# Optimization experiments

Hardware: AMD Instinct MI355X
Metric: run time of the kernel (lower is better)

## Reference

```python
import jax, jax.numpy as jnp
import numpy as np

G, C_PER, C_IN, J, B, H, W, K = 8, 32, 256, 64, 16, 56, 56, 3


def setup_inputs() -> dict:
    key = jax.random.key(0)
    kx, kw, kb = jax.random.split(key, 3)
    x = jax.random.normal(kx, (B, C_IN, H, W), dtype=jnp.float32)
    # Per-cluster conv weights [G, j_rank, c, K, K] and biases [G, j_rank]
    weight = jax.random.normal(kw, (G, J, C_PER, K, K), dtype=jnp.float32) * 0.05
    bias = jax.random.normal(kb, (G, J), dtype=jnp.float32) * 0.01
    # Arrangements: 8 clusters of 32 non-contiguous channel indices (fixed permutation)
    arrangements = jnp.asarray(
        np.random.RandomState(0).permutation(C_IN).reshape(G, C_PER), dtype=jnp.int32
    )
    return {"x": x, "weight": weight, "bias": bias, "arrangements": arrangements}


def reference(x, weight, bias, arrangements):
    # Gather channel subsets: x[:, arr] -> [B, G, c, H, W] -> [G, B, c, H, W]
    xg = jnp.transpose(x[:, arrangements], (1, 0, 2, 3, 4))

    def conv1(xi, wi):
        # xi: [B, c, H, W], wi: [J, c, K, K]; stride 1, pad 1, dilation 1 (torch default cross-correlation)
        return jax.lax.conv_general_dilated(
            xi, wi,
            window_strides=(1, 1),
            padding=((1, 1), (1, 1)),
            dimension_numbers=("NCHW", "OIHW", "NCHW"),
        )

    out = jax.vmap(conv1)(xg, weight)              # [G, B, J, H, W]
    out = out + bias[:, None, :, None, None]
    g, b, j, h, w = out.shape
    # torch.cat(dim=1) over clusters -> [B, G*J, H, W]
    return jnp.transpose(out, (1, 0, 2, 3, 4)).reshape(b, g * j, h, w)
```

## Files before the change

kernel.cpp:

```cpp
#include <hip/hip_runtime.h>


#define NG 8
#define CPER 32
#define CIN 256
#define NJ 64
#define NB 16
#define NH 56
#define NW 56
#define HW (NH * NW)
#define PLANE_DW 236
#define SLOT_DW 944
#define NSLOT 6
#define BUF_DW (NSLOT * SLOT_DW)
#define NTASK 336

typedef __attribute__((ext_vector_type(8))) short short8v;
typedef __attribute__((ext_vector_type(4))) float float4v;
typedef __attribute__((ext_vector_type(4))) unsigned int uint4v;

__device__ __forceinline__ unsigned bf16rne(float f) {
    unsigned u = __float_as_uint(f);
    return (u + 0x7FFFu + ((u >> 16) & 1u)) >> 16;
}

#define MFMA __builtin_amdgcn_mfma_f32_16x16x32_bf16

__global__ __launch_bounds__(256)
void transpose_w(const float* __restrict__ w, unsigned short* __restrict__ wt) {
    const int idx = blockIdx.x * 256 + threadIdx.x;
    const float* src = w + (size_t)idx * 9;
    const int g = idx >> 11, jc = idx & 2047;
    #pragma unroll
    for (int t = 0; t < 9; ++t)
        wt[(g * 9 + t) * 2048 + jc] = (unsigned short)bf16rne(src[t]);
}

__global__ __launch_bounds__(256, 4)
void gconv_mfma(const float* __restrict__ x,
                const unsigned short* __restrict__ wt,
                const float* __restrict__ bias,
                const int* __restrict__ arr,
                float* __restrict__ out) {
    __shared__ __align__(16) unsigned int smw[BUF_DW];

    const int tid   = threadIdx.x;
    const int chunk = blockIdx.x;
    const int b     = blockIdx.y;
    const int g     = blockIdx.z;
    const int lane  = tid & 63;
    const int jt    = tid >> 6;
    const int n     = lane & 15;
    const int kq    = lane >> 4;
    const int rbase = chunk * 4;

    short8v A[9];
    {
        const unsigned short* wl =
            wt + (size_t)(g * 9) * 2048 + (jt * 16 + n) * CPER + kq * 8;
        #pragma unroll
        for (int t = 0; t < 9; ++t)
            A[t] = *(const short8v*)(wl + t * 2048);
    }
    float4v binit;
    #pragma unroll
    for (int i = 0; i < 4; ++i) binit[i] = bias[g * NJ + jt * 16 + kq * 4 + i];

    if (tid < 48) {
        int lr = tid >> 3, rm = tid & 7;
        int q = rm >> 1, px = (rm & 1) ? 57 : 0;
        uint4v z = {0u, 0u, 0u, 0u};
        *(uint4v*)(smw + lr * SLOT_DW + q * PLANE_DW + px * 4) = z;
    }

    const float* xb = x + (size_t)b * (CIN * HW);
    const int* ag = arr + g * CPER;
    auto stage = [&](int t) {
        int q = t & 3, s = t >> 2;
        int p4 = s % 14, lr = s / 14;
        int irow = rbase - 1 + lr;
        bool v = (unsigned)irow < NH;
        const float* src = xb + irow * NW + 4 * p4;
        float4v vv[8];
        #pragma unroll
        for (int j = 0; j < 8; ++j) {
            float4v t0 = {0.f, 0.f, 0.f, 0.f};
            if (v) t0 = *(const float4v*)(src + ag[8 * q + j] * HW);
            vv[j] = t0;
        }
        unsigned int* d = smw + lr * SLOT_DW + q * PLANE_DW + (1 + 4 * p4) * 4;
        #pragma unroll
        for (int i = 0; i < 4; ++i) {
            uint4v val;
            #pragma unroll
            for (int dd = 0; dd < 4; ++dd)
                val[dd] = bf16rne(vv[2 * dd][i]) | (bf16rne(vv[2 * dd + 1][i]) << 16);
            *(uint4v*)(d + 4 * i) = val;
        }
    };
    stage(tid);
    if (tid < NTASK - 256) stage(tid + 256);
    __syncthreads();

    const int ob = ((b * (NG * NJ) + g * NJ + jt * 16 + kq * 4) * NH + rbase) * NW;
    int rl = 0, col = n;
    #pragma unroll
    for (int tp = 0; tp < 7; ++tp) {
        const int rlA = rl, colA = col;
        col += 16; if (col >= NW) { col -= NW; ++rl; }
        const int rlB = rl, colB = col;
        col += 16; if (col >= NW) { col -= NW; ++rl; }
        const unsigned int* pA = smw + rlA * SLOT_DW + kq * PLANE_DW + colA * 4;
        const unsigned int* pB = smw + rlB * SLOT_DW + kq * PLANE_DW + colB * 4;
        float4v a0 = binit, a1 = binit;
        #pragma unroll
        for (int kh = 0; kh < 3; ++kh)
            #pragma unroll
            for (int kw = 0; kw < 3; ++kw) {
                short8v x0 = *(const short8v*)(pA + kh * SLOT_DW + kw * 4);
                short8v y0 = *(const short8v*)(pB + kh * SLOT_DW + kw * 4);
                a0 = MFMA(A[kh * 3 + kw], x0, a0, 0, 0, 0);
                a1 = MFMA(A[kh * 3 + kw], y0, a1, 0, 0, 0);
            }
        const int oA = ob + rlA * NW + colA;
        const int oB = ob + rlB * NW + colB;
        #pragma unroll
        for (int i = 0; i < 4; ++i) {
            out[oA + i * HW] = a0[i];
            out[oB + i * HW] = a1[i];
        }
    }
}

extern "C" void kernel_launch(void* const* d_in, const int* in_sizes, int n_in,
                              void* d_out, int out_size, void* d_ws, size_t ws_size,
                              hipStream_t stream) {
    const float* x    = (const float*)d_in[0];
    const float* wght = (const float*)d_in[1];
    const float* bias = (const float*)d_in[2];
    const int*   arr  = (const int*)d_in[3];
    float* out = (float*)d_out;
    unsigned short* wtp = (unsigned short*)d_ws;

    transpose_w<<<dim3(64), 256, 0, stream>>>(wght, wtp);
    dim3 grid(14, NB, NG);
    gconv_mfma<<<grid, 256, 0, stream>>>(x, wtp, bias, arr, out);
}
```

Before: 169.3 us.

## Split waves over two output-channel tiles and two row halves for B-fragment reuse

Each wave now computes two 16-channel output tiles for half of the block's pixels (2 rows × 56), instead of one channel tile for all 4 rows. Every LDS-loaded input fragment now feeds two MFMAs, which halves shared-memory read traffic per MFMA. In exchange each wave holds twice the weight registers (18 short8 fragments) and four accumulators, which raises VGPR pressure and may hurt occupancy under launch_bounds(256,4). A tail step handles the seventh 16-pixel tile of each half.

```diff
diff --git a/kernel.cpp b/kernel.cpp
--- a/kernel.cpp
+++ b/kernel.cpp
@@ -49,22 +49,28 @@
     const int b     = blockIdx.y;
     const int g     = blockIdx.z;
     const int lane  = tid & 63;
-    const int jt    = tid >> 6;
+    const int wid   = tid >> 6;
     const int n     = lane & 15;
     const int kq    = lane >> 4;
+    const int jt0   = (wid & 1) * 2;
+    const int ph    = wid >> 1;
     const int rbase = chunk * 4;
 
-    short8v A[9];
-    {
+    short8v A[2][9];
+    #pragma unroll
+    for (int jj = 0; jj < 2; ++jj) {
         const unsigned short* wl =
-            wt + (size_t)(g * 9) * 2048 + (jt * 16 + n) * CPER + kq * 8;
+            wt + (size_t)(g * 9) * 2048 + ((jt0 + jj) * 16 + n) * CPER + kq * 8;
         #pragma unroll
         for (int t = 0; t < 9; ++t)
-            A[t] = *(const short8v*)(wl + t * 2048);
+            A[jj][t] = *(const short8v*)(wl + t * 2048);
     }
-    float4v binit;
+    float4v binit[2];
     #pragma unroll
-    for (int i = 0; i < 4; ++i) binit[i] = bias[g * NJ + jt * 16 + kq * 4 + i];
+    for (int jj = 0; jj < 2; ++jj)
+        #pragma unroll
+        for (int i = 0; i < 4; ++i)
+            binit[jj][i] = bias[g * NJ + (jt0 + jj) * 16 + kq * 4 + i];
 
     if (tid < 48) {
         int lr = tid >> 3, rm = tid & 7;
@@ -102,33 +108,55 @@
     if (tid < NTASK - 256) stage(tid + 256);
     __syncthreads();
 
-    const int ob = ((b * (NG * NJ) + g * NJ + jt * 16 + kq * 4) * NH + rbase) * NW;
-    int rl = 0, col = n;
+    const int ob0 = ((b * (NG * NJ) + g * NJ + jt0 * 16 + kq * 4) * NH + rbase) * NW;
+    const int ob1 = ob0 + 16 * HW;
+    int rl = 2 * ph, col = n;
     #pragma unroll
-    for (int tp = 0; tp < 7; ++tp) {
+    for (int tp = 0; tp < 3; ++tp) {
         const int rlA = rl, colA = col;
         col += 16; if (col >= NW) { col -= NW; ++rl; }
         const int rlB = rl, colB = col;
         col += 16; if (col >= NW) { col -= NW; ++rl; }
         const unsigned int* pA = smw + rlA * SLOT_DW + kq * PLANE_DW + colA * 4;
         const unsigned int* pB = smw + rlB * SLOT_DW + kq * PLANE_DW + colB * 4;
-        float4v a0 = binit, a1 = binit;
+        float4v a00 = binit[0], a01 = binit[1];
+        float4v a10 = binit[0], a11 = binit[1];
         #pragma unroll
         for (int kh = 0; kh < 3; ++kh)
             #pragma unroll
             for (int kw = 0; kw < 3; ++kw) {
                 short8v x0 = *(const short8v*)(pA + kh * SLOT_DW + kw * 4);
                 short8v y0 = *(const short8v*)(pB + kh * SLOT_DW + kw * 4);
-                a0 = MFMA(A[kh * 3 + kw], x0, a0, 0, 0, 0);
-                a1 = MFMA(A[kh * 3 + kw], y0, a1, 0, 0, 0);
+                a00 = MFMA(A[0][kh * 3 + kw], x0, a00, 0, 0, 0);
+                a01 = MFMA(A[1][kh * 3 + kw], x0, a01, 0, 0, 0);
+                a10 = MFMA(A[0][kh * 3 + kw], y0, a10, 0, 0, 0);
+                a11 = MFMA(A[1][kh * 3 + kw], y0, a11, 0, 0, 0);
             }
-        const int oA = ob + rlA * NW + colA;
-        const int oB = ob + rlB * NW + colB;
+        const int oA = rlA * NW + colA;
+        const int oB = rlB * NW + colB;
         #pragma unroll
         for (int i = 0; i < 4; ++i) {
-            out[oA + i * HW] = a0[i];
-            out[oB + i * HW] = a1[i];
+            out[ob0 + oA + i * HW] = a00[i];
+            out[ob1 + oA + i * HW] = a01[i];
+            out[ob0 + oB + i * HW] = a10[i];
+            out[ob1 + oB + i * HW] = a11[i];
         }
+    }
+    const unsigned int* pA = smw + rl * SLOT_DW + kq * PLANE_DW + col * 4;
+    float4v a00 = binit[0], a01 = binit[1];
+    #pragma unroll
+    for (int kh = 0; kh < 3; ++kh)
+        #pragma unroll
+        for (int kw = 0; kw < 3; ++kw) {
+            short8v x0 = *(const short8v*)(pA + kh * SLOT_DW + kw * 4);
+            a00 = MFMA(A[0][kh * 3 + kw], x0, a00, 0, 0, 0);
+            a01 = MFMA(A[1][kh * 3 + kw], x0, a01, 0, 0, 0);
+        }
+    const int oA = rl * NW + col;
+    #pragma unroll
+    for (int i = 0; i < 4; ++i) {
+        out[ob0 + oA + i * HW] = a00[i];
+        out[ob1 + oA + i * HW] = a01[i];
     }
 }
 
```

Result: slower. 200.7 us (+18.6%).
